# Optimization experiments

Hardware: AMD Instinct MI355X
Metric: run time of the kernel (lower is better)

## Reference

```python
import jax, jax.numpy as jnp
import numpy as np

D = 128  # vector dimension (must be multiple of 8)


def pack_signs_to_uint8(signs):
    """signs: (..., D) of +/-1 floats -> (..., D//8) uint8, bit i = element 8j+i of byte j."""
    bits = (signs > 0).astype(jnp.uint8).reshape(*signs.shape[:-1], D // 8, 8)
    weights = jnp.left_shift(jnp.uint8(1), jnp.arange(8, dtype=jnp.uint8))  # [1,2,...,128]
    return jnp.sum(bits * weights, axis=-1).astype(jnp.uint8)


def unpack_signs_from_uint8(packed):
    """packed: (..., D//8) uint8 -> (..., D) float32 of +/-1."""
    shifts = jnp.arange(8, dtype=jnp.uint8)
    bits = jnp.bitwise_and(jnp.right_shift(packed[..., None], shifts), jnp.uint8(1))  # (..., D//8, 8)
    signs = bits.astype(jnp.float32) * 2.0 - 1.0
    return signs.reshape(*packed.shape[:-1], D)


def setup_inputs() -> dict:
    key = jax.random.key(0)
    kx, = jax.random.split(key, 1)
    x = jax.random.normal(kx, (4, 16, 4096, D), dtype=jnp.float32)
    # Full random rotation buffer: QR of seeded gaussian (seed=42), as in __init__.
    rng = np.random.default_rng(42)
    A = rng.standard_normal((D, D)).astype(np.float64)
    Q, _ = np.linalg.qr(A)
    P = jnp.asarray(Q, dtype=jnp.float32)
    return {"x": x, "P": P}


def reference(x, P):
    """RaBitQ forward: quantize -> dequantize round trip.
    Returns (x_hat, packed_signs, norms_fp16, x0_fp16)."""
    # ---- quantize ----
    norms = jnp.maximum(jnp.linalg.norm(x, axis=-1), 1e-8)        # (B,H,S)
    x_unit = x / norms[..., None]
    x_rot = jnp.einsum('bhsd,ed->bhse', x_unit, P)                # x_unit @ P.T
    signs = jnp.where(x_rot >= 0, 1.0, -1.0)                      # sign with 0 -> +1
    x0 = jnp.sum(x_rot * signs, axis=-1) / D                      # alignment = mean |x_rot|
    packed = pack_signs_to_uint8(signs)                           # (B,H,S,D//8) uint8
    norms16 = norms.astype(jnp.float16)
    x016 = x0.astype(jnp.float16)
    # ---- dequantize ----
    signs_u = unpack_signs_from_uint8(packed)                     # (B,H,S,D)
    x_rot_approx = signs_u * x016.astype(jnp.float32)[..., None]
    x_unit_approx = jnp.einsum('bhsd,de->bhse', x_rot_approx, P)  # @ P (inverse rotation)
    x_hat = x_unit_approx * norms16.astype(jnp.float32)[..., None]
    return x_hat, packed, norms16, x016
```

## Files before the change

### kernel.cpp

```cpp
#include <hip/hip_runtime.h>
#include <hip/hip_fp16.h>


#define NVEC_TOTAL (4 * 16 * 4096)
#define ROUNDS 4

typedef short short8 __attribute__((ext_vector_type(8)));
typedef float f32x4 __attribute__((ext_vector_type(4)));
typedef unsigned int u32x4v __attribute__((ext_vector_type(4)));
typedef unsigned long long ull;

__device__ __forceinline__ float rfl_f(float v) {
  return __int_as_float(__builtin_amdgcn_readfirstlane(__float_as_int(v)));
}

__device__ __forceinline__ ull sel8_u64(const ull* a, int s) {
  ull r0 = (s & 1) ? a[1] : a[0];
  ull r1 = (s & 1) ? a[3] : a[2];
  ull r2 = (s & 1) ? a[5] : a[4];
  ull r3 = (s & 1) ? a[7] : a[6];
  ull r4 = (s & 2) ? r1 : r0;
  ull r5 = (s & 2) ? r3 : r2;
  return (s & 4) ? r5 : r4;
}

__device__ __forceinline__ float sel8_f(const float* a, int s) {
  float r0 = (s & 1) ? a[1] : a[0];
  float r1 = (s & 1) ? a[3] : a[2];
  float r2 = (s & 1) ? a[5] : a[4];
  float r3 = (s & 1) ? a[7] : a[6];
  float r4 = (s & 2) ? r1 : r0;
  float r5 = (s & 2) ? r3 : r2;
  return (s & 4) ? r5 : r4;
}

__device__ __forceinline__ unsigned short f2bf(float f) {
  unsigned u = __float_as_uint(f);
  return (unsigned short)((u + 0x7FFFu + ((u >> 16) & 1u)) >> 16);
}

__global__ __launch_bounds__(1024, 4) void rabitq_quant(const float* __restrict__ x,
                                                        const float* __restrict__ Pm,
                                                        float* __restrict__ out) {
  extern __shared__ __align__(16) char smem[];
  float* const Pl = (float*)smem;
  char* const xs = smem + 65536;

  const int tid = threadIdx.x;
  const int lane = tid & 63;
  const int ww = tid >> 6;

  {
    const int r = tid >> 3;
    const int q = tid & 7;
#pragma unroll
    for (int c = 0; c < 4; ++c) {
      const int dd = q * 16 + c * 4;
      const int sj = (((dd >> 2) ^ (r & 7)) << 2);
      const float4 v = *(const float4*)(Pm + (size_t)r * 128 + dd);
      *(float4*)(&Pl[r * 128 + sj]) = v;
    }
  }
  __syncthreads();

  const int w = blockIdx.x * 16 + ww;
  float* const out_pack = out + (size_t)NVEC_TOTAL * 128;
  float* const out_norm = out_pack + (size_t)NVEC_TOTAL * 16;
  float* const out_x0   = out_norm + NVEC_TOTAL;

  const int sw1 = lane & 7;
  float* const xb = (float*)(xs + ww * 4096);
  const int lsub = (lane >> 5);
  const int lcol = (lane & 31) * 4;

  float4 pf0, pf1, pf2, pf3;
  {
    const int vb = w * 32;
    pf0 = *(const float4*)(x + (size_t)(vb + 0 + lsub) * 128 + lcol);
    pf1 = *(const float4*)(x + (size_t)(vb + 2 + lsub) * 128 + lcol);
    pf2 = *(const float4*)(x + (size_t)(vb + 4 + lsub) * 128 + lcol);
    pf3 = *(const float4*)(x + (size_t)(vb + 6 + lsub) * 128 + lcol);
  }

#pragma unroll 1
  for (int t = 0; t < ROUNDS; ++t) {
    const int vbase = w * 32 + t * 8;

    {
      char* const dst = (char*)xb + lane * 16;
      *(float4*)(dst + 0)    = pf0;
      *(float4*)(dst + 1024) = pf1;
      *(float4*)(dst + 2048) = pf2;
      *(float4*)(dst + 3072) = pf3;
    }

    if (t + 1 < ROUNDS) {
      const int vb = w * 32 + (t + 1) * 8;
      pf0 = *(const float4*)(x + (size_t)(vb + 0 + lsub) * 128 + lcol);
      pf1 = *(const float4*)(x + (size_t)(vb + 2 + lsub) * 128 + lcol);
      pf2 = *(const float4*)(x + (size_t)(vb + 4 + lsub) * 128 + lcol);
      pf3 = *(const float4*)(x + (size_t)(vb + 6 + lsub) * 128 + lcol);
    }

    float acc_lo[8], acc_hi[8];
#pragma unroll
    for (int v = 0; v < 8; ++v) { acc_lo[v] = 0.f; acc_hi[v] = 0.f; }

#pragma unroll 2
    for (int j = 0; j < 32; ++j) {
      const int js = ((j ^ sw1) << 2);
      const float4 pl = *(const float4*)(&Pl[lane * 128 + js]);
      const float4 ph = *(const float4*)(&Pl[(lane + 64) * 128 + js]);
#pragma unroll
      for (int v = 0; v < 8; ++v) {
        const float4 xv = *(const float4*)(xb + v * 128 + j * 4);
        float al = acc_lo[v], ah = acc_hi[v];
        al = fmaf(xv.x, pl.x, al); ah = fmaf(xv.x, ph.x, ah);
        al = fmaf(xv.y, pl.y, al); ah = fmaf(xv.y, ph.y, ah);
        al = fmaf(xv.z, pl.z, al); ah = fmaf(xv.z, ph.z, ah);
        al = fmaf(xv.w, pl.w, al); ah = fmaf(xv.w, ph.w, ah);
        acc_lo[v] = al; acc_hi[v] = ah;
      }
    }

    ull bl[8], bh[8];
    float n16v[8], x0v[8];
#pragma unroll
    for (int v = 0; v < 8; ++v) {
      bl[v] = __ballot(acc_lo[v] >= 0.0f);
      bh[v] = __ballot(acc_hi[v] >= 0.0f);
      const float a1 = fabsf(acc_lo[v]);
      const float a2 = fabsf(acc_hi[v]);
      float s1 = a1 + a2;
      float n2 = fmaf(a1, a1, a2 * a2);
#pragma unroll
      for (int off = 32; off > 0; off >>= 1) {
        s1 += __shfl_xor(s1, off);
        n2 += __shfl_xor(n2, off);
      }
      float norm = fmaxf(sqrtf(n2), 1e-8f);
      const float n16  = __half2float(__float2half(norm));
      const float x0   = s1 / (128.0f * norm);
      const float x016 = __half2float(__float2half(x0));
      n16v[v] = rfl_f(n16);
      x0v[v]  = rfl_f(x016);
    }

    {
      const int s = lane & 7;
      const int jb = lane >> 3;
      const ull el = sel8_u64(bl, s);
      const ull eh = sel8_u64(bh, s);
      const float fl = (float)((unsigned)(el >> (8 * jb)) & 255u);
      const float fh = (float)((unsigned)(eh >> (8 * jb)) & 255u);
      out_pack[(size_t)(vbase + s) * 16 + jb] = fl;
      out_pack[(size_t)(vbase + s) * 16 + 8 + jb] = fh;
      if (lane < 16) {
        const float nsel = sel8_f(n16v, s);
        const float xsel = sel8_f(x0v, s);
        if (lane < 8) out_norm[vbase + s] = nsel;
        else          out_x0[vbase + s] = xsel;
      }
    }
  }
}

__global__ __launch_bounds__(256, 4) void rabitq_dequant(const float* __restrict__ Pm,
                                                         float* __restrict__ out) {
  __shared__ __align__(16) unsigned Bp[2048 * 4];

  const int tid = threadIdx.x, lane = tid & 63, ww = tid >> 6;
  const int l15 = lane & 15, lg = lane >> 4;

#pragma unroll
  for (int i = 0; i < 8; ++i) {
    const int s = tid + i * 256;
    const int ks = s >> 9, n = (s >> 6) & 7, l = s & 63;
    const int kb = ks * 32 + (l >> 4) * 8;
    const int f = n * 16 + (l & 15);
    u32x4v wv;
#pragma unroll
    for (int u = 0; u < 4; ++u) {
      const float p0 = Pm[(size_t)(kb + 2 * u) * 128 + f];
      const float p1 = Pm[(size_t)(kb + 2 * u + 1) * 128 + f];
      wv[u] = (unsigned)f2bf(p0) | ((unsigned)f2bf(p1) << 16);
    }
    *(u32x4v*)(&Bp[s * 4]) = wv;
  }
  __syncthreads();

  const float* const out_pack = out + (size_t)NVEC_TOTAL * 128;
  const float* const out_norm = out_pack + (size_t)NVEC_TOTAL * 16;
  const float* const out_x0   = out_norm + NVEC_TOTAL;

#pragma unroll 1
  for (int t = 0; t < 4; ++t) {
    const int vbase = (blockIdx.x * 4 + ww) * 64 + t * 16;
    const int vec = vbase + l15;

    const float* pb = out_pack + (size_t)vec * 16;
    const float4 b0 = *(const float4*)(pb + 0);
    const float4 b1 = *(const float4*)(pb + 4);
    const float4 b2 = *(const float4*)(pb + 8);
    const float4 b3 = *(const float4*)(pb + 12);
    unsigned mw[4];
    mw[0] = (unsigned)b0.x | ((unsigned)b0.y << 8) | ((unsigned)b0.z << 16) | ((unsigned)b0.w << 24);
    mw[1] = (unsigned)b1.x | ((unsigned)b1.y << 8) | ((unsigned)b1.z << 16) | ((unsigned)b1.w << 24);
    mw[2] = (unsigned)b2.x | ((unsigned)b2.y << 8) | ((unsigned)b2.z << 16) | ((unsigned)b2.w << 24);
    mw[3] = (unsigned)b3.x | ((unsigned)b3.y << 8) | ((unsigned)b3.z << 16) | ((unsigned)b3.w << 24);

    short8 a8[4];
#pragma unroll
    for (int ks = 0; ks < 4; ++ks) {
      const unsigned nb = (~mw[ks]) >> (lg * 8);
      u32x4v ta;
      ta[0] = 0x3F803F80u | ((nb & 1u) << 15)        | ((nb & 2u) << 30);
      ta[1] = 0x3F803F80u | (((nb >> 2) & 1u) << 15) | (((nb >> 2) & 2u) << 30);
      ta[2] = 0x3F803F80u | (((nb >> 4) & 1u) << 15) | (((nb >> 4) & 2u) << 30);
      ta[3] = 0x3F803F80u | (((nb >> 6) & 1u) << 15) | (((nb >> 6) & 2u) << 30);
      a8[ks] = __builtin_bit_cast(short8, ta);
    }

    f32x4 dacc[8];
#pragma unroll
    for (int n = 0; n < 8; ++n) { dacc[n][0] = 0.f; dacc[n][1] = 0.f; dacc[n][2] = 0.f; dacc[n][3] = 0.f; }
#pragma unroll
    for (int n = 0; n < 8; ++n) {
#pragma unroll
      for (int ks = 0; ks < 4; ++ks) {
        const short8 b8 = __builtin_bit_cast(short8, *(const u32x4v*)(&Bp[(ks * 512 + n * 64 + lane) * 4]));
        dacc[n] = __builtin_amdgcn_mfma_f32_16x16x32_bf16(a8[ks], b8, dacc[n], 0, 0, 0);
      }
    }

#pragma unroll
    for (int r = 0; r < 4; ++r) {
      const int row = vbase + lg * 4 + r;
      const float sc = out_norm[row] * out_x0[row];
      float* op = out + (size_t)row * 128 + l15;
#pragma unroll
      for (int n = 0; n < 8; ++n) op[n * 16] = sc * dacc[n][r];
    }
  }
}

extern "C" void kernel_launch(void* const* d_in, const int* in_sizes, int n_in,
                              void* d_out, int out_size, void* d_ws, size_t ws_size,
                              hipStream_t stream) {
  const float* x  = (const float*)d_in[0];
  const float* Pm = (const float*)d_in[1];
  float* out = (float*)d_out;
  hipLaunchKernelGGL(rabitq_quant, dim3(512), dim3(1024), 131072, stream, x, Pm, out);
  hipLaunchKernelGGL(rabitq_dequant, dim3(1024), dim3(256), 0, stream, Pm, out);
}
```

Before: 243.0 us.

## Fuse quantize and dequantize into one kernel with register-resident signs

Merges the separate quantize and dequantize kernels into one. Sign ballots and scale factors stay in registers and feed the MFMA inverse rotation directly, so the dequant pass no longer re-reads the packed signs, norms and x0 from global memory. The bf16 B fragments of P are built once by a small one-block prep kernel into workspace and read from global/L2 inside the MFMA loop instead of LDS. It also replaces the shuffle reductions with DPP/swizzle wave sums. The costs are more register pressure in the 1024-thread blocks and an extra serial launch.

```diff
diff --git a/kernel.cpp b/kernel.cpp
--- a/kernel.cpp
+++ b/kernel.cpp
@@ -3,7 +3,6 @@
 
 
 #define NVEC_TOTAL (4 * 16 * 4096)
-#define ROUNDS 4
 
 typedef short short8 __attribute__((ext_vector_type(8)));
 typedef float f32x4 __attribute__((ext_vector_type(4)));
@@ -34,13 +33,62 @@
   return (s & 4) ? r5 : r4;
 }
 
+__device__ __forceinline__ ull sel16_u64(const ull* a, int s) {
+  ull lo = sel8_u64(a, s);
+  ull hi = sel8_u64(a + 8, s);
+  return (s & 8) ? hi : lo;
+}
+
+__device__ __forceinline__ float sel16_f(const float* a, int s) {
+  float lo = sel8_f(a, s);
+  float hi = sel8_f(a + 8, s);
+  return (s & 8) ? hi : lo;
+}
+
+template <int CTRL>
+__device__ __forceinline__ float dpp_add(float v) {
+  int t = __builtin_amdgcn_update_dpp(0, __float_as_int(v), CTRL, 0xF, 0xF, true);
+  return v + __int_as_float(t);
+}
+
+__device__ __forceinline__ float wave_sum(float v) {
+  v = dpp_add<0x121>(v);
+  v = dpp_add<0x122>(v);
+  v = dpp_add<0x124>(v);
+  v = dpp_add<0x128>(v);
+  v += __int_as_float(__builtin_amdgcn_ds_swizzle(__float_as_int(v), 0x401F));
+  v += __shfl_xor(v, 32);
+  return v;
+}
+
 __device__ __forceinline__ unsigned short f2bf(float f) {
   unsigned u = __float_as_uint(f);
   return (unsigned short)((u + 0x7FFFu + ((u >> 16) & 1u)) >> 16);
 }
 
-__global__ __launch_bounds__(1024, 4) void rabitq_quant(const float* __restrict__ x,
+__global__ __launch_bounds__(256, 4) void prep_bfrags(const float* __restrict__ Pm,
+                                                      unsigned* __restrict__ ws) {
+  const int tid = threadIdx.x;
+#pragma unroll
+  for (int i = 0; i < 8; ++i) {
+    const int s = tid + i * 256;
+    const int ks = s >> 9, n = (s >> 6) & 7, l = s & 63;
+    const int kb = ks * 32 + (l >> 4) * 8;
+    const int f = n * 16 + (l & 15);
+    u32x4v wv;
+#pragma unroll
+    for (int u = 0; u < 4; ++u) {
+      const float p0 = Pm[(size_t)(kb + 2 * u) * 128 + f];
+      const float p1 = Pm[(size_t)(kb + 2 * u + 1) * 128 + f];
+      wv[u] = (unsigned)f2bf(p0) | ((unsigned)f2bf(p1) << 16);
+    }
+    *(u32x4v*)(ws + s * 4) = wv;
+  }
+}
+
+__global__ __launch_bounds__(1024, 4) void rabitq_fused(const float* __restrict__ x,
                                                         const float* __restrict__ Pm,
+                                                        const unsigned* __restrict__ bw,
                                                         float* __restrict__ out) {
   extern __shared__ __align__(16) char smem[];
   float* const Pl = (float*)smem;
@@ -49,6 +97,7 @@
   const int tid = threadIdx.x;
   const int lane = tid & 63;
   const int ww = tid >> 6;
+  const int l15 = lane & 15, lg = lane >> 4;
 
   {
     const int r = tid >> 3;
@@ -82,132 +131,99 @@
     pf3 = *(const float4*)(x + (size_t)(vb + 6 + lsub) * 128 + lcol);
   }
 
-#pragma unroll 1
-  for (int t = 0; t < ROUNDS; ++t) {
-    const int vbase = w * 32 + t * 8;
-
-    {
-      char* const dst = (char*)xb + lane * 16;
-      *(float4*)(dst + 0)    = pf0;
-      *(float4*)(dst + 1024) = pf1;
-      *(float4*)(dst + 2048) = pf2;
-      *(float4*)(dst + 3072) = pf3;
-    }
-
-    if (t + 1 < ROUNDS) {
-      const int vb = w * 32 + (t + 1) * 8;
-      pf0 = *(const float4*)(x + (size_t)(vb + 0 + lsub) * 128 + lcol);
-      pf1 = *(const float4*)(x + (size_t)(vb + 2 + lsub) * 128 + lcol);
-      pf2 = *(const float4*)(x + (size_t)(vb + 4 + lsub) * 128 + lcol);
-      pf3 = *(const float4*)(x + (size_t)(vb + 6 + lsub) * 128 + lcol);
-    }
-
-    float acc_lo[8], acc_hi[8];
-#pragma unroll
-    for (int v = 0; v < 8; ++v) { acc_lo[v] = 0.f; acc_hi[v] = 0.f; }
+#pragma unroll
+  for (int g = 0; g < 2; ++g) {
+    ull gL[16], gH[16];
+    float gSc[16];
+
+#pragma unroll
+    for (int p = 0; p < 2; ++p) {
+      const int t = g * 2 + p;
+      const int vbase = w * 32 + t * 8;
+
+      {
+        char* const dst = (char*)xb + lane * 16;
+        *(float4*)(dst + 0)    = pf0;
+        *(float4*)(dst + 1024) = pf1;
+        *(float4*)(dst + 2048) = pf2;
+        *(float4*)(dst + 3072) = pf3;
+      }
+
+      if (t + 1 < 4) {
+        const int vb = w * 32 + (t + 1) * 8;
+        pf0 = *(const float4*)(x + (size_t)(vb + 0 + lsub) * 128 + lcol);
+        pf1 = *(const float4*)(x + (size_t)(vb + 2 + lsub) * 128 + lcol);
+        pf2 = *(const float4*)(x + (size_t)(vb + 4 + lsub) * 128 + lcol);
+        pf3 = *(const float4*)(x + (size_t)(vb + 6 + lsub) * 128 + lcol);
+      }
+
+      float acc_lo[8], acc_hi[8];
+#pragma unroll
+      for (int v = 0; v < 8; ++v) { acc_lo[v] = 0.f; acc_hi[v] = 0.f; }
 
 #pragma unroll 2
-    for (int j = 0; j < 32; ++j) {
-      const int js = ((j ^ sw1) << 2);
-      const float4 pl = *(const float4*)(&Pl[lane * 128 + js]);
-      const float4 ph = *(const float4*)(&Pl[(lane + 64) * 128 + js]);
+      for (int j = 0; j < 32; ++j) {
+        const int js = ((j ^ sw1) << 2);
+        const float4 pl = *(const float4*)(&Pl[lane * 128 + js]);
+        const float4 ph = *(const float4*)(&Pl[(lane + 64) * 128 + js]);
+#pragma unroll
+        for (int v = 0; v < 8; ++v) {
+          const float4 xv = *(const float4*)(xb + v * 128 + j * 4);
+          float al = acc_lo[v], ah = acc_hi[v];
+          al = fmaf(xv.x, pl.x, al); ah = fmaf(xv.x, ph.x, ah);
+          al = fmaf(xv.y, pl.y, al); ah = fmaf(xv.y, ph.y, ah);
+          al = fmaf(xv.z, pl.z, al); ah = fmaf(xv.z, ph.z, ah);
+          al = fmaf(xv.w, pl.w, al); ah = fmaf(xv.w, ph.w, ah);
+          acc_lo[v] = al; acc_hi[v] = ah;
+        }
+      }
+
+      ull abl[8], abh[8];
+      float n16v[8], x0v[8];
 #pragma unroll
       for (int v = 0; v < 8; ++v) {
-        const float4 xv = *(const float4*)(xb + v * 128 + j * 4);
-        float al = acc_lo[v], ah = acc_hi[v];
-        al = fmaf(xv.x, pl.x, al); ah = fmaf(xv.x, ph.x, ah);
-        al = fmaf(xv.y, pl.y, al); ah = fmaf(xv.y, ph.y, ah);
-        al = fmaf(xv.z, pl.z, al); ah = fmaf(xv.z, ph.z, ah);
-        al = fmaf(xv.w, pl.w, al); ah = fmaf(xv.w, ph.w, ah);
-        acc_lo[v] = al; acc_hi[v] = ah;
-      }
-    }
-
-    ull bl[8], bh[8];
-    float n16v[8], x0v[8];
-#pragma unroll
-    for (int v = 0; v < 8; ++v) {
-      bl[v] = __ballot(acc_lo[v] >= 0.0f);
-      bh[v] = __ballot(acc_hi[v] >= 0.0f);
-      const float a1 = fabsf(acc_lo[v]);
-      const float a2 = fabsf(acc_hi[v]);
-      float s1 = a1 + a2;
-      float n2 = fmaf(a1, a1, a2 * a2);
-#pragma unroll
-      for (int off = 32; off > 0; off >>= 1) {
-        s1 += __shfl_xor(s1, off);
-        n2 += __shfl_xor(n2, off);
-      }
-      float norm = fmaxf(sqrtf(n2), 1e-8f);
-      const float n16  = __half2float(__float2half(norm));
-      const float x0   = s1 / (128.0f * norm);
-      const float x016 = __half2float(__float2half(x0));
-      n16v[v] = rfl_f(n16);
-      x0v[v]  = rfl_f(x016);
-    }
-
-    {
-      const int s = lane & 7;
-      const int jb = lane >> 3;
-      const ull el = sel8_u64(bl, s);
-      const ull eh = sel8_u64(bh, s);
-      const float fl = (float)((unsigned)(el >> (8 * jb)) & 255u);
-      const float fh = (float)((unsigned)(eh >> (8 * jb)) & 255u);
-      out_pack[(size_t)(vbase + s) * 16 + jb] = fl;
-      out_pack[(size_t)(vbase + s) * 16 + 8 + jb] = fh;
-      if (lane < 16) {
-        const float nsel = sel8_f(n16v, s);
-        const float xsel = sel8_f(x0v, s);
-        if (lane < 8) out_norm[vbase + s] = nsel;
-        else          out_x0[vbase + s] = xsel;
-      }
-    }
-  }
-}
-
-__global__ __launch_bounds__(256, 4) void rabitq_dequant(const float* __restrict__ Pm,
-                                                         float* __restrict__ out) {
-  __shared__ __align__(16) unsigned Bp[2048 * 4];
-
-  const int tid = threadIdx.x, lane = tid & 63, ww = tid >> 6;
-  const int l15 = lane & 15, lg = lane >> 4;
-
-#pragma unroll
-  for (int i = 0; i < 8; ++i) {
-    const int s = tid + i * 256;
-    const int ks = s >> 9, n = (s >> 6) & 7, l = s & 63;
-    const int kb = ks * 32 + (l >> 4) * 8;
-    const int f = n * 16 + (l & 15);
-    u32x4v wv;
-#pragma unroll
-    for (int u = 0; u < 4; ++u) {
-      const float p0 = Pm[(size_t)(kb + 2 * u) * 128 + f];
-      const float p1 = Pm[(size_t)(kb + 2 * u + 1) * 128 + f];
-      wv[u] = (unsigned)f2bf(p0) | ((unsigned)f2bf(p1) << 16);
-    }
-    *(u32x4v*)(&Bp[s * 4]) = wv;
-  }
-  __syncthreads();
-
-  const float* const out_pack = out + (size_t)NVEC_TOTAL * 128;
-  const float* const out_norm = out_pack + (size_t)NVEC_TOTAL * 16;
-  const float* const out_x0   = out_norm + NVEC_TOTAL;
-
-#pragma unroll 1
-  for (int t = 0; t < 4; ++t) {
-    const int vbase = (blockIdx.x * 4 + ww) * 64 + t * 16;
-    const int vec = vbase + l15;
-
-    const float* pb = out_pack + (size_t)vec * 16;
-    const float4 b0 = *(const float4*)(pb + 0);
-    const float4 b1 = *(const float4*)(pb + 4);
-    const float4 b2 = *(const float4*)(pb + 8);
-    const float4 b3 = *(const float4*)(pb + 12);
+        abl[v] = __ballot(acc_lo[v] >= 0.0f);
+        abh[v] = __ballot(acc_hi[v] >= 0.0f);
+        const float a1 = fabsf(acc_lo[v]);
+        const float a2 = fabsf(acc_hi[v]);
+        const float s1 = wave_sum(a1 + a2);
+        const float n2 = wave_sum(fmaf(a1, a1, a2 * a2));
+        const float norm = fmaxf(sqrtf(n2), 1e-8f);
+        const float n16  = __half2float(__float2half(norm));
+        const float x0   = s1 / (128.0f * norm);
+        const float x016 = __half2float(__float2half(x0));
+        n16v[v] = rfl_f(n16);
+        x0v[v]  = rfl_f(x016);
+        gL[p * 8 + v] = abl[v];
+        gH[p * 8 + v] = abh[v];
+        gSc[p * 8 + v] = rfl_f(n16 * x016);
+      }
+
+      {
+        const int s = lane & 7;
+        const int jb = lane >> 3;
+        const ull el = sel8_u64(abl, s);
+        const ull eh = sel8_u64(abh, s);
+        const float fl = (float)((unsigned)(el >> (8 * jb)) & 255u);
+        const float fh = (float)((unsigned)(eh >> (8 * jb)) & 255u);
+        out_pack[(size_t)(vbase + s) * 16 + jb] = fl;
+        out_pack[(size_t)(vbase + s) * 16 + 8 + jb] = fh;
+        if (lane < 16) {
+          const float nsel = sel8_f(n16v, s);
+          const float xsel = sel8_f(x0v, s);
+          if (lane < 8) out_norm[vbase + s] = nsel;
+          else          out_x0[vbase + s] = xsel;
+        }
+      }
+    }
+
+    const int gvb = w * 32 + g * 16;
+
+    const ull selL = sel16_u64(gL, l15);
+    const ull selH = sel16_u64(gH, l15);
     unsigned mw[4];
-    mw[0] = (unsigned)b0.x | ((unsigned)b0.y << 8) | ((unsigned)b0.z << 16) | ((unsigned)b0.w << 24);
-    mw[1] = (unsigned)b1.x | ((unsigned)b1.y << 8) | ((unsigned)b1.z << 16) | ((unsigned)b1.w << 24);
-    mw[2] = (unsigned)b2.x | ((unsigned)b2.y << 8) | ((unsigned)b2.z << 16) | ((unsigned)b2.w << 24);
-    mw[3] = (unsigned)b3.x | ((unsigned)b3.y << 8) | ((unsigned)b3.z << 16) | ((unsigned)b3.w << 24);
+    mw[0] = (unsigned)selL; mw[1] = (unsigned)(selL >> 32);
+    mw[2] = (unsigned)selH; mw[3] = (unsigned)(selH >> 32);
 
     short8 a8[4];
 #pragma unroll
@@ -228,18 +244,19 @@
     for (int n = 0; n < 8; ++n) {
 #pragma unroll
       for (int ks = 0; ks < 4; ++ks) {
-        const short8 b8 = __builtin_bit_cast(short8, *(const u32x4v*)(&Bp[(ks * 512 + n * 64 + lane) * 4]));
+        const short8 b8 = __builtin_bit_cast(short8, *(const u32x4v*)(bw + (size_t)(ks * 512 + n * 64 + lane) * 4));
         dacc[n] = __builtin_amdgcn_mfma_f32_16x16x32_bf16(a8[ks], b8, dacc[n], 0, 0, 0);
       }
     }
 
+    float sc[4];
+#pragma unroll
+    for (int r = 0; r < 4; ++r) sc[r] = sel16_f(gSc, lg * 4 + r);
 #pragma unroll
     for (int r = 0; r < 4; ++r) {
-      const int row = vbase + lg * 4 + r;
-      const float sc = out_norm[row] * out_x0[row];
-      float* op = out + (size_t)row * 128 + l15;
-#pragma unroll
-      for (int n = 0; n < 8; ++n) op[n * 16] = sc * dacc[n][r];
+      float* op = out + (size_t)(gvb + lg * 4 + r) * 128 + l15;
+#pragma unroll
+      for (int n = 0; n < 8; ++n) op[n * 16] = sc[r] * dacc[n][r];
     }
   }
 }
@@ -250,6 +267,7 @@
   const float* x  = (const float*)d_in[0];
   const float* Pm = (const float*)d_in[1];
   float* out = (float*)d_out;
-  hipLaunchKernelGGL(rabitq_quant, dim3(512), dim3(1024), 131072, stream, x, Pm, out);
-  hipLaunchKernelGGL(rabitq_dequant, dim3(1024), dim3(256), 0, stream, Pm, out);
-}
+  hipLaunchKernelGGL(prep_bfrags, dim3(1), dim3(256), 0, stream, Pm, (unsigned*)d_ws);
+  hipLaunchKernelGGL(rabitq_fused, dim3(512), dim3(1024), 131072, stream,
+                     x, Pm, (const unsigned*)d_ws, out);
+}
```

Measured after the change: 340.4 us. 1.4x slower.
